# Kernel optimization log

Hardware: AMD Instinct MI355X
Metric: run time of the kernel (lower is better)

## Reference

```python
import jax, jax.numpy as jnp
import numpy as np
from jax import lax

B, CIN, H, W = 32, 128, 64, 64
COUT, K, NK, HID = 128, 3, 4, 32
TEMP = 34.0
PAD = 1


def setup_inputs() -> dict:
    key = jax.random.key(0)
    k1, k2, k3, k4 = jax.random.split(key, 4)
    x = jax.random.normal(k1, (B, CIN, H, W), dtype=jnp.float32)
    fc1_w = jax.random.normal(k2, (HID, CIN), dtype=jnp.float32) * (2.0 / CIN) ** 0.5
    fc2_w = jax.random.normal(k3, (NK, HID), dtype=jnp.float32) * (2.0 / HID) ** 0.5
    fc2_b = jnp.zeros((NK,), dtype=jnp.float32)
    weight = jax.random.normal(k4, (NK, COUT, CIN, K, K), dtype=jnp.float32) * 0.05
    bias = jnp.zeros((NK, COUT), dtype=jnp.float32)
    return {"x": x, "fc1_w": fc1_w, "fc2_w": fc2_w, "fc2_b": fc2_b,
            "weight": weight, "bias": bias}


def _per_sample_conv(xi, wi):
    # xi: [CIN, H, W], wi: [COUT, CIN, K, K]
    out = lax.conv_general_dilated(
        xi[None], wi,
        window_strides=(1, 1),
        padding=[(PAD, PAD), (PAD, PAD)],
        dimension_numbers=("NCHW", "OIHW", "NCHW"))
    return out[0]  # [COUT, H', W']


def reference(x, fc1_w, fc2_w, fc2_b, weight, bias):
    # attention: global avg pool -> 1x1 conv (matmul) -> relu -> 1x1 conv -> softmax
    context = jnp.mean(x, axis=(2, 3))                      # [B, CIN]
    hid = jax.nn.relu(context @ fc1_w.T)                    # [B, HID]
    logits = hid @ fc2_w.T + fc2_b                          # [B, NK]
    att = jax.nn.softmax(logits / TEMP, axis=1)             # [B, NK]
    # aggregate per-sample kernels and biases
    agg_w = jnp.einsum("bk,koihw->boihw", att, weight)      # [B, COUT, CIN, K, K]
    agg_b = att @ bias                                      # [B, COUT]
    # per-sample convolution (equivalent to the groups=B trick in torch)
    out = jax.vmap(_per_sample_conv)(x, agg_w)              # [B, COUT, H, W]
    return out + agg_b[:, :, None, None]
```

## Files before the change

### kernel.cpp

```cpp
#include <hip/hip_runtime.h>
#include <hip/hip_bf16.h>

#define B_    32
#define CIN_  128
#define H_    64
#define W_    64
#define COUT_ 128
#define NK_   4
#define HID_  32
#define TEMP_ 34.0f

typedef short bf16x8 __attribute__((ext_vector_type(8)));
typedef short short4v __attribute__((ext_vector_type(4)));
typedef float f32x4  __attribute__((ext_vector_type(4)));
typedef float f32x16 __attribute__((ext_vector_type(16)));

__device__ __forceinline__ short f2bf(float f) {
    union { float f; unsigned u; } c; c.f = f;
    unsigned r = (c.u + 0x7FFFu + ((c.u >> 16) & 1u)) >> 16;
    return (short)r;
}
__device__ __forceinline__ float bf2f(short s) {
    union { unsigned u; float f; } c; c.u = ((unsigned)(unsigned short)s) << 16;
    return c.f;
}

#define TPAD 140
__global__ __launch_bounds__(256) void k_prep(const float* __restrict__ x,
                                              float* __restrict__ ctx,
                                              short* __restrict__ xb) {
    __shared__ short T[64 * TPAD];
    const int tid = threadIdx.x;
    const int b = blockIdx.x >> 6;
    const int h = blockIdx.x & 63;
    const int w = tid & 63;
    const int wv = tid >> 6;
    const float* xp = x + (size_t)b * CIN_ * (H_ * W_) + h * W_ + w;
#pragma unroll
    for (int j = 0; j < 8; ++j) {
        const int ci0 = j * 16 + wv * 4;
        float v0 = xp[(size_t)(ci0 + 0) * (H_ * W_)];
        float v1 = xp[(size_t)(ci0 + 1) * (H_ * W_)];
        float v2 = xp[(size_t)(ci0 + 2) * (H_ * W_)];
        float v3 = xp[(size_t)(ci0 + 3) * (H_ * W_)];
        short4v sv = { f2bf(v0), f2bf(v1), f2bf(v2), f2bf(v3) };
        *(short4v*)(&T[w * TPAD + ci0]) = sv;
    }
    __syncthreads();
    {
        const int ci = tid >> 1;
        const int ph = tid & 1;
        float s = 0.f;
        for (int ww = ph * 32; ww < ph * 32 + 32; ++ww) s += bf2f(T[ww * TPAD + ci]);
        s += __shfl_down(s, 1, 64);
        if (ph == 0) atomicAdd(&ctx[b * CIN_ + ci], s);
    }
    const int ww = tid >> 2;
    const int cc = tid & 3;
    short* op = xb + (((size_t)b * H_ + h) * W_ + ww) * CIN_ + cc * 32;
    const short* tp = &T[ww * TPAD + cc * 32];
#pragma unroll
    for (int k = 0; k < 4; ++k)
        *(bf16x8*)(op + k * 8) = *(const bf16x8*)(tp + k * 8);
}

__global__ void k_context(const float* __restrict__ x, float* __restrict__ ctx) {
    const int bc = blockIdx.x;
    const float* p = x + (size_t)bc * (H_ * W_);
    const int lane = threadIdx.x;
    float s = 0.f;
    for (int i = lane * 4; i < H_ * W_; i += 64 * 4) {
        float4 v = *(const float4*)(p + i);
        s += v.x + v.y + v.z + v.w;
    }
    for (int off = 32; off > 0; off >>= 1) s += __shfl_down(s, off, 64);
    if (lane == 0) ctx[bc] = s * (1.0f / (H_ * W_));
}

#define SF1S 129
__global__ __launch_bounds__(1024) void k_att(const float* __restrict__ ctx,
                      const float* __restrict__ fc1w,
                      const float* __restrict__ fc2w,
                      const float* __restrict__ fc2b,
                      const float* __restrict__ bias,
                      float* __restrict__ att, float* __restrict__ aggb,
                      float ctx_scale) {
    __shared__ float sctx[B_ * CIN_];
    __shared__ float sf1[HID_ * SF1S];
    __shared__ float shid[B_ * HID_];
    __shared__ float satt[B_ * NK_];
    const int t = threadIdx.x;
    for (int i = t; i < B_ * CIN_; i += 1024) sctx[i] = ctx[i] * ctx_scale;
    for (int i = t; i < HID_ * CIN_; i += 1024) sf1[(i >> 7) * SF1S + (i & 127)] = fc1w[i];
    __syncthreads();
    {
        const int b = t >> 5, hh = t & 31;
        float s = 0.f;
        for (int ci = 0; ci < CIN_; ++ci) s += sctx[b * CIN_ + ci] * sf1[hh * SF1S + ci];
        shid[b * HID_ + hh] = fmaxf(s, 0.f);
    }
    __syncthreads();
    if (t < B_) {
        float lg[NK_]; float mx = -1e30f;
#pragma unroll
        for (int k = 0; k < NK_; ++k) {
            float s = fc2b[k];
            for (int hh = 0; hh < HID_; ++hh) s += shid[t * HID_ + hh] * fc2w[k * HID_ + hh];
            lg[k] = s / TEMP_; mx = fmaxf(mx, lg[k]);
        }
        float den = 0.f;
#pragma unroll
        for (int k = 0; k < NK_; ++k) { lg[k] = expf(lg[k] - mx); den += lg[k]; }
        const float rd = 1.0f / den;
#pragma unroll
        for (int k = 0; k < NK_; ++k) { satt[t * NK_ + k] = lg[k] * rd; att[t * NK_ + k] = lg[k] * rd; }
    }
    __syncthreads();
    {
        const int b = t >> 5, c0 = (t & 31) * 4;
        float4 bw[NK_];
#pragma unroll
        for (int k = 0; k < NK_; ++k) bw[k] = *(const float4*)(bias + k * COUT_ + c0);
        float4 r = make_float4(0.f, 0.f, 0.f, 0.f);
#pragma unroll
        for (int k = 0; k < NK_; ++k) {
            const float a = satt[b * NK_ + k];
            r.x += a * bw[k].x; r.y += a * bw[k].y; r.z += a * bw[k].z; r.w += a * bw[k].w;
        }
        *(float4*)(aggb + b * COUT_ + c0) = r;
    }
}

__global__ void k_aggw(const float* __restrict__ att,
                       const float* __restrict__ weight,
                       short* __restrict__ aggwt) {
    const int idx = blockIdx.x * 256 + threadIdx.x;
    const int ci = idx & 127;
    const int co = (idx >> 7) & 127;
    const int b  = idx >> 14;
    const float a0 = att[b * NK_ + 0];
    const float a1 = att[b * NK_ + 1];
    const float a2 = att[b * NK_ + 2];
    const float a3 = att[b * NK_ + 3];
    const float* w0 = weight + ((size_t)co * CIN_ + ci) * 9;
    const float* w1 = w0 + (size_t)COUT_ * CIN_ * 9;
    const float* w2 = w1 + (size_t)COUT_ * CIN_ * 9;
    const float* w3 = w2 + (size_t)COUT_ * CIN_ * 9;
    short* o = aggwt + ((size_t)(b * COUT_ + co) * 9) * CIN_ + ci;
#pragma unroll
    for (int r = 0; r < 9; ++r)
        o[r * CIN_] = f2bf(a0 * w0[r] + a1 * w1[r] + a2 * w2[r] + a3 * w3[r]);
}

#define RCH 528
#define RBY 8448
__global__ __launch_bounds__(256, 4) void k_conv(const short* __restrict__ xb,
        const short* __restrict__ aggwt, const float* __restrict__ aggb,
        float* __restrict__ out) {
    __shared__ short xt[4 * RCH * 8];
    const int tid = threadIdx.x;
    const int blk = blockIdx.x;
    const int b = blk & 31;
    const int h0 = (blk >> 5) * 2;
    const int lane = tid & 63;
    const int wv = tid >> 6;
    const int l31 = lane & 31;
    const int lane5 = lane >> 5;

    const int in_h = h0 - 1 + wv;
    const bool valid = (in_h >= 0) && (in_h < H_);
    short* rowp = &xt[wv * (RBY / 2)];
    if (!valid) {
        for (int j = 0; j < 9; ++j) {
            const int idx = j * 64 + lane;
            if (idx < RCH) *(int4*)(&rowp[idx * 8]) = make_int4(0, 0, 0, 0);
        }
    } else if (lane < 16) {
        const int cl = (lane < 8) ? lane : (512 + lane);
        *(int4*)(&rowp[cl * 8]) = make_int4(0, 0, 0, 0);
    }

    f32x16 acc[4];
#pragma unroll
    for (int nt = 0; nt < 4; ++nt)
#pragma unroll
        for (int k = 0; k < 16; ++k) acc[nt][k] = 0.f;

    const short* Ap = aggwt + (size_t)(b * COUT_ + wv * 32 + l31) * 9 * CIN_ + lane5 * 8;

    for (int half = 0; half < 2; ++half) {
        if (valid) {
            const size_t gband = ((size_t)b * H_ + in_h) * W_;
#pragma unroll
            for (int j = 0; j < 8; ++j) {
                const int cl = 8 + j * 64 + lane;
                const int s = cl >> 3;
                const int p = cl & 7;
                const int wp = s - 1;
                const int ci8 = half * 8 + ((p - wp) & 7);
                const short* gp = xb + (gband + wp) * CIN_ + ci8 * 8;
                __builtin_amdgcn_global_load_lds(
                    (const __attribute__((address_space(1))) void*)gp,
                    (__attribute__((address_space(3))) void*)(rowp + (8 + j * 64) * 8),
                    16, 0, 0);
            }
        }
        __syncthreads();

#pragma unroll
        for (int kcl = 0; kcl < 4; ++kcl) {
            const int kc = half * 4 + kcl;
            int SB[2][3];
#pragma unroll
            for (int i = 0; i < 2; ++i)
#pragma unroll
                for (int kw = 0; kw < 3; ++kw) {
                    const int s = i * 32 + l31 + kw;
                    SB[i][kw] = s * 128 + 16 * ((2 * kcl + lane5 + s - 1) & 7);
                }
#pragma unroll
            for (int r = 0; r < 9; ++r) {
                const int kh = r / 3, kw = r % 3;
                bf16x8 av = *(const bf16x8*)(Ap + kc * 16 + r * CIN_);
#pragma unroll
                for (int nt = 0; nt < 4; ++nt) {
                    const char* bp = (const char*)xt + SB[nt & 1][kw] + ((nt >> 1) + kh) * RBY;
                    bf16x8 bv = *(const bf16x8*)bp;
                    acc[nt] = __builtin_amdgcn_mfma_f32_32x32x16_bf16(av, bv, acc[nt], 0, 0, 0);
                }
            }
        }
        if (half == 0) __syncthreads();
    }

    const float* ab = aggb + b * COUT_;
#pragma unroll
    for (int nt = 0; nt < 4; ++nt) {
        const int hh = h0 + (nt >> 1);
        const int w = (nt & 1) * 32 + l31;
        float* op = out + ((size_t)b * COUT_ * H_ + hh) * W_ + w;
#pragma unroll
        for (int reg = 0; reg < 16; ++reg) {
            const int co = wv * 32 + (reg & 3) + 8 * (reg >> 2) + 4 * lane5;
            op[(size_t)co * (H_ * W_)] = acc[nt][reg] + ab[co];
        }
    }
}

#define LDS_S 136
__global__ __launch_bounds__(256) void k_conv_fb(const float* __restrict__ x,
                                              const short* __restrict__ aggwt,
                                              const float* __restrict__ aggb,
                                              float* __restrict__ out) {
    __shared__ short xs[3 * 66 * LDS_S];
    const int tid = threadIdx.x;
    const int b = blockIdx.x >> 6;
    const int h = blockIdx.x & 63;
    for (int i = tid; i < 3 * 32 * 16; i += 256) {
        const int hr  = i >> 9;
        const int rem = i & 511;
        const int ci4 = rem >> 4;
        const int wb  = rem & 15;
        const int ih = h + hr - 1;
        float4 v0 = make_float4(0.f, 0.f, 0.f, 0.f), v1 = v0, v2 = v0, v3 = v0;
        if (ih >= 0 && ih < H_) {
            const float* base = x + (((size_t)b * CIN_ + ci4 * 4) * H_ + ih) * W_ + wb * 4;
            v0 = *(const float4*)(base);
            v1 = *(const float4*)(base + H_ * W_);
            v2 = *(const float4*)(base + 2 * H_ * W_);
            v3 = *(const float4*)(base + 3 * H_ * W_);
        }
        short* p = &xs[(hr * 66 + 1 + wb * 4) * LDS_S + ci4 * 4];
        short4v s0 = { f2bf(v0.x), f2bf(v1.x), f2bf(v2.x), f2bf(v3.x) };
        short4v s1 = { f2bf(v0.y), f2bf(v1.y), f2bf(v2.y), f2bf(v3.y) };
        short4v s2 = { f2bf(v0.z), f2bf(v1.z), f2bf(v2.z), f2bf(v3.z) };
        short4v s3 = { f2bf(v0.w), f2bf(v1.w), f2bf(v2.w), f2bf(v3.w) };
        *(short4v*)(p + 0 * LDS_S) = s0;
        *(short4v*)(p + 1 * LDS_S) = s1;
        *(short4v*)(p + 2 * LDS_S) = s2;
        *(short4v*)(p + 3 * LDS_S) = s3;
        short4v z = { 0, 0, 0, 0 };
        if (wb == 0)  *(short4v*)(&xs[(hr * 66 + 0) * LDS_S + ci4 * 4]) = z;
        if (wb == 15) *(short4v*)(&xs[(hr * 66 + 65) * LDS_S + ci4 * 4]) = z;
    }
    __syncthreads();
    const int lane = tid & 63;
    const int wave = tid >> 6;
    const int quad = lane >> 4;
    const int l16  = lane & 15;
    f32x4 acc[2][4];
#pragma unroll
    for (int i = 0; i < 2; ++i)
#pragma unroll
        for (int j = 0; j < 4; ++j) acc[i][j] = (f32x4){0.f, 0.f, 0.f, 0.f};
    const short* A0 = aggwt + (size_t)(b * COUT_ + wave * 32 + l16) * 9 * CIN_;
    const short* A1 = A0 + 16 * 9 * CIN_;
    for (int r = 0; r < 9; ++r) {
        const int kh = r / 3, kw = r % 3;
#pragma unroll
        for (int c = 0; c < 4; ++c) {
            const int k0 = c * 32 + quad * 8;
            bf16x8 a0 = *(const bf16x8*)(A0 + r * CIN_ + k0);
            bf16x8 a1 = *(const bf16x8*)(A1 + r * CIN_ + k0);
#pragma unroll
            for (int nt = 0; nt < 4; ++nt) {
                const int col = nt * 16 + l16 + kw;
                bf16x8 bv = *(const bf16x8*)(&xs[(kh * 66 + col) * LDS_S + k0]);
                acc[0][nt] = __builtin_amdgcn_mfma_f32_16x16x32_bf16(a0, bv, acc[0][nt], 0, 0, 0);
                acc[1][nt] = __builtin_amdgcn_mfma_f32_16x16x32_bf16(a1, bv, acc[1][nt], 0, 0, 0);
            }
        }
    }
    float* outb = out + (size_t)b * COUT_ * H_ * W_ + h * W_;
    const float* ab = aggb + b * COUT_;
#pragma unroll
    for (int mt = 0; mt < 2; ++mt)
#pragma unroll
        for (int rr = 0; rr < 4; ++rr) {
            const int co = wave * 32 + mt * 16 + quad * 4 + rr;
            const float bb = ab[co];
#pragma unroll
            for (int nt = 0; nt < 4; ++nt)
                outb[(size_t)co * (H_ * W_) + nt * 16 + l16] = acc[mt][nt][rr] + bb;
        }
}

extern "C" void kernel_launch(void* const* d_in, const int* in_sizes, int n_in,
                              void* d_out, int out_size, void* d_ws, size_t ws_size,
                              hipStream_t stream) {
    const float* x    = (const float*)d_in[0];
    const float* fc1w = (const float*)d_in[1];
    const float* fc2w = (const float*)d_in[2];
    const float* fc2b = (const float*)d_in[3];
    const float* wgt  = (const float*)d_in[4];
    const float* bias = (const float*)d_in[5];
    float* out = (float*)d_out;

    char* ws = (char*)d_ws;
    float* ctx   = (float*)(ws + 0);
    float* att   = (float*)(ws + 16384);
    float* aggb  = (float*)(ws + 16896);
    short* aggwt = (short*)(ws + 65536);
    short* xb    = (short*)(ws + 9502720);
    const size_t NEED = 9502720u + 33554432u;

    if (ws_size >= NEED) {
        hipMemsetAsync(ctx, 0, B_ * CIN_ * sizeof(float), stream);
        k_prep<<<dim3(B_ * H_), dim3(256), 0, stream>>>(x, ctx, xb);
        k_att<<<dim3(1), dim3(1024), 0, stream>>>(ctx, fc1w, fc2w, fc2b, bias, att, aggb,
                                                  1.0f / (H_ * W_));
        k_aggw<<<dim3((B_ * COUT_ * CIN_) / 256), dim3(256), 0, stream>>>(att, wgt, aggwt);
        k_conv<<<dim3(B_ * (H_ / 2)), dim3(256), 0, stream>>>(xb, aggwt, aggb, out);
    } else {
        k_context<<<dim3(B_ * CIN_), dim3(64), 0, stream>>>(x, ctx);
        k_att<<<dim3(1), dim3(1024), 0, stream>>>(ctx, fc1w, fc2w, fc2b, bias, att, aggb, 1.0f);
        k_aggw<<<dim3((B_ * COUT_ * CIN_) / 256), dim3(256), 0, stream>>>(att, wgt, aggwt);
        k_conv_fb<<<dim3(B_ * H_), dim3(256), 0, stream>>>(x, aggwt, aggb, out);
    }
}
```

Measured before the change: 194.6 us.

## Compute four output rows per conv block and vectorize prep loads

The conv kernel now covers 4 output rows per block instead of 2, staging 6 input rows in LDS. Each staged B fragment is reused across up to 3 output rows, and all 9 A fragments are held in registers per channel chunk. This cuts LDS reads and the halo reload overhead, at the cost of twice the accumulators (8 tiles), fewer blocks per CU (launch bound lowered to 2) and half the grid. The prep kernel now reads x with coalesced float4 loads along width and does scattered 2-byte LDS stores for the transpose.

```diff
diff --git a/kernel.cpp b/kernel.cpp
--- a/kernel.cpp
+++ b/kernel.cpp
@@ -33,18 +33,17 @@
     const int tid = threadIdx.x;
     const int b = blockIdx.x >> 6;
     const int h = blockIdx.x & 63;
-    const int w = tid & 63;
-    const int wv = tid >> 6;
-    const float* xp = x + (size_t)b * CIN_ * (H_ * W_) + h * W_ + w;
-#pragma unroll
-    for (int j = 0; j < 8; ++j) {
-        const int ci0 = j * 16 + wv * 4;
-        float v0 = xp[(size_t)(ci0 + 0) * (H_ * W_)];
-        float v1 = xp[(size_t)(ci0 + 1) * (H_ * W_)];
-        float v2 = xp[(size_t)(ci0 + 2) * (H_ * W_)];
-        float v3 = xp[(size_t)(ci0 + 3) * (H_ * W_)];
-        short4v sv = { f2bf(v0), f2bf(v1), f2bf(v2), f2bf(v3) };
-        *(short4v*)(&T[w * TPAD + ci0]) = sv;
+#pragma unroll
+    for (int k = 0; k < 8; ++k) {
+        const int idx = k * 256 + tid;
+        const int wq = idx & 15;
+        const int ci = idx >> 4;
+        float4 v = *(const float4*)(x + (((size_t)b * CIN_ + ci) * H_ + h) * W_ + wq * 4);
+        short* p = &T[(wq * 4) * TPAD + ci];
+        p[0 * TPAD] = f2bf(v.x);
+        p[1 * TPAD] = f2bf(v.y);
+        p[2 * TPAD] = f2bf(v.z);
+        p[3 * TPAD] = f2bf(v.w);
     }
     __syncthreads();
     {
@@ -152,57 +151,56 @@
         o[r * CIN_] = f2bf(a0 * w0[r] + a1 * w1[r] + a2 * w2[r] + a3 * w3[r]);
 }
 
-#define RCH 528
 #define RBY 8448
-__global__ __launch_bounds__(256, 4) void k_conv(const short* __restrict__ xb,
+#define RSH 4224
+__global__ __launch_bounds__(256, 2) void k_conv(const short* __restrict__ xb,
         const short* __restrict__ aggwt, const float* __restrict__ aggb,
         float* __restrict__ out) {
-    __shared__ short xt[4 * RCH * 8];
+    __shared__ short xt[6 * RSH];
     const int tid = threadIdx.x;
     const int blk = blockIdx.x;
     const int b = blk & 31;
-    const int h0 = (blk >> 5) * 2;
+    const int h0 = (blk >> 5) * 4;
     const int lane = tid & 63;
     const int wv = tid >> 6;
     const int l31 = lane & 31;
     const int lane5 = lane >> 5;
 
-    const int in_h = h0 - 1 + wv;
-    const bool valid = (in_h >= 0) && (in_h < H_);
-    short* rowp = &xt[wv * (RBY / 2)];
-    if (!valid) {
-        for (int j = 0; j < 9; ++j) {
-            const int idx = j * 64 + lane;
-            if (idx < RCH) *(int4*)(&rowp[idx * 8]) = make_int4(0, 0, 0, 0);
-        }
-    } else if (lane < 16) {
-        const int cl = (lane < 8) ? lane : (512 + lane);
-        *(int4*)(&rowp[cl * 8]) = make_int4(0, 0, 0, 0);
-    }
-
-    f32x16 acc[4];
-#pragma unroll
-    for (int nt = 0; nt < 4; ++nt)
-#pragma unroll
-        for (int k = 0; k < 16; ++k) acc[nt][k] = 0.f;
+    if (tid < 96) {
+        const int row = tid >> 4;
+        const int q = tid & 15;
+        const int cl = (q < 8) ? q : (512 + q);
+        *(int4*)(&xt[row * RSH + cl * 8]) = make_int4(0, 0, 0, 0);
+    }
+
+    f32x16 acc[8];
+#pragma unroll
+    for (int t = 0; t < 8; ++t)
+#pragma unroll
+        for (int k = 0; k < 16; ++k) acc[t][k] = 0.f;
 
     const short* Ap = aggwt + (size_t)(b * COUT_ + wv * 32 + l31) * 9 * CIN_ + lane5 * 8;
 
     for (int half = 0; half < 2; ++half) {
-        if (valid) {
-            const size_t gband = ((size_t)b * H_ + in_h) * W_;
-#pragma unroll
-            for (int j = 0; j < 8; ++j) {
-                const int cl = 8 + j * 64 + lane;
+#pragma unroll
+        for (int k = 0; k < 12; ++k) {
+            const int cbase = k * 256 + wv * 64;
+            const int row = cbase >> 9;
+            const int clb = (cbase & 511) + 8;
+            const int in_h = h0 - 1 + row;
+            short* dst = &xt[row * RSH + clb * 8];
+            if (in_h >= 0 && in_h < H_) {
+                const int cl = clb + lane;
                 const int s = cl >> 3;
                 const int p = cl & 7;
                 const int wp = s - 1;
                 const int ci8 = half * 8 + ((p - wp) & 7);
-                const short* gp = xb + (gband + wp) * CIN_ + ci8 * 8;
+                const short* gp = xb + (((size_t)b * H_ + in_h) * W_ + wp) * CIN_ + ci8 * 8;
                 __builtin_amdgcn_global_load_lds(
                     (const __attribute__((address_space(1))) void*)gp,
-                    (__attribute__((address_space(3))) void*)(rowp + (8 + j * 64) * 8),
-                    16, 0, 0);
+                    (__attribute__((address_space(3))) void*)dst, 16, 0, 0);
+            } else {
+                *(int4*)(dst + lane * 8) = make_int4(0, 0, 0, 0);
             }
         }
         __syncthreads();
@@ -210,23 +208,32 @@
 #pragma unroll
         for (int kcl = 0; kcl < 4; ++kcl) {
             const int kc = half * 4 + kcl;
-            int SB[2][3];
-#pragma unroll
-            for (int i = 0; i < 2; ++i)
-#pragma unroll
-                for (int kw = 0; kw < 3; ++kw) {
-                    const int s = i * 32 + l31 + kw;
-                    SB[i][kw] = s * 128 + 16 * ((2 * kcl + lane5 + s - 1) & 7);
-                }
-#pragma unroll
-            for (int r = 0; r < 9; ++r) {
-                const int kh = r / 3, kw = r % 3;
-                bf16x8 av = *(const bf16x8*)(Ap + kc * 16 + r * CIN_);
-#pragma unroll
-                for (int nt = 0; nt < 4; ++nt) {
-                    const char* bp = (const char*)xt + SB[nt & 1][kw] + ((nt >> 1) + kh) * RBY;
-                    bf16x8 bv = *(const bf16x8*)bp;
-                    acc[nt] = __builtin_amdgcn_mfma_f32_32x32x16_bf16(av, bv, acc[nt], 0, 0, 0);
+            bf16x8 av[9];
+#pragma unroll
+            for (int r = 0; r < 9; ++r)
+                av[r] = *(const bf16x8*)(Ap + kc * 16 + r * CIN_);
+#pragma unroll
+            for (int ir = 0; ir < 6; ++ir) {
+                bf16x8 bv[2][3];
+#pragma unroll
+                for (int i = 0; i < 2; ++i)
+#pragma unroll
+                    for (int kw = 0; kw < 3; ++kw) {
+                        const int s = i * 32 + l31 + kw;
+                        const int off = 16 * ((2 * kcl + lane5 + s - 1) & 7);
+                        bv[i][kw] = *(const bf16x8*)((const char*)xt + ir * RBY + s * 128 + off);
+                    }
+#pragma unroll
+                for (int orr = 0; orr < 4; ++orr) {
+                    if (orr <= ir && ir <= orr + 2) {
+                        const int kh = ir - orr;
+#pragma unroll
+                        for (int i = 0; i < 2; ++i)
+#pragma unroll
+                            for (int kw = 0; kw < 3; ++kw)
+                                acc[orr * 2 + i] = __builtin_amdgcn_mfma_f32_32x32x16_bf16(
+                                    av[kh * 3 + kw], bv[i][kw], acc[orr * 2 + i], 0, 0, 0);
+                    }
                 }
             }
         }
@@ -235,14 +242,18 @@
 
     const float* ab = aggb + b * COUT_;
 #pragma unroll
-    for (int nt = 0; nt < 4; ++nt) {
-        const int hh = h0 + (nt >> 1);
-        const int w = (nt & 1) * 32 + l31;
-        float* op = out + ((size_t)b * COUT_ * H_ + hh) * W_ + w;
-#pragma unroll
-        for (int reg = 0; reg < 16; ++reg) {
-            const int co = wv * 32 + (reg & 3) + 8 * (reg >> 2) + 4 * lane5;
-            op[(size_t)co * (H_ * W_)] = acc[nt][reg] + ab[co];
+    for (int orr = 0; orr < 4; ++orr) {
+#pragma unroll
+        for (int i = 0; i < 2; ++i) {
+            const int hh = h0 + orr;
+            const int w = i * 32 + l31;
+            float* op = out + ((size_t)b * COUT_ * H_ + hh) * W_ + w;
+            const f32x16 a = acc[orr * 2 + i];
+#pragma unroll
+            for (int reg = 0; reg < 16; ++reg) {
+                const int co = wv * 32 + (reg & 3) + 8 * (reg >> 2) + 4 * lane5;
+                op[(size_t)co * (H_ * W_)] = a[reg] + ab[co];
+            }
         }
     }
 }
@@ -350,7 +361,7 @@
         k_att<<<dim3(1), dim3(1024), 0, stream>>>(ctx, fc1w, fc2w, fc2b, bias, att, aggb,
                                                   1.0f / (H_ * W_));
         k_aggw<<<dim3((B_ * COUT_ * CIN_) / 256), dim3(256), 0, stream>>>(att, wgt, aggwt);
-        k_conv<<<dim3(B_ * (H_ / 2)), dim3(256), 0, stream>>>(xb, aggwt, aggb, out);
+        k_conv<<<dim3(B_ * (H_ / 4)), dim3(256), 0, stream>>>(xb, aggwt, aggb, out);
     } else {
         k_context<<<dim3(B_ * CIN_), dim3(64), 0, stream>>>(x, ctx);
         k_att<<<dim3(1), dim3(1024), 0, stream>>>(ctx, fc1w, fc2w, fc2b, bias, att, aggb, 1.0f);
```

Result: no change. 192.5 us (-1.1%).
